# Kernel optimization log

Measured on AMD Instinct MI355X. Metric: run time of the kernel, lower is better.

The kernel has to match this reference:

```python
import jax, jax.numpy as jnp
import numpy as np

EPS = 1e-12
B, H, W, DIN = 32, 32, 32, 1024
DE = 64          # embedding_dim
K = 8192         # num_embeddings
S = 16           # code_seq_len -> 4x4 adaptive pool grid
GH = GW = 4


def setup_inputs() -> dict:
    key = jax.random.key(0)
    ks = jax.random.split(key, 8)
    return {
        "features_t0": jax.random.normal(ks[0], (B, H, W, DIN), dtype=jnp.float32),
        "features_t1": jax.random.normal(ks[1], (B, H, W, DIN), dtype=jnp.float32),
        "noise": jax.random.normal(ks[2], (B * S, DE), dtype=jnp.float32),
        "codebooks": jax.random.normal(ks[3], (K, DE), dtype=jnp.float32),
        "W_in": jax.random.normal(ks[4], (DE, DIN), dtype=jnp.float32) / np.sqrt(DIN),
        "b_in": jnp.zeros((DE,), dtype=jnp.float32),
        "W_out": jax.random.normal(ks[5], (DIN, DE), dtype=jnp.float32) / np.sqrt(DE),
        "b_out": jnp.zeros((DIN,), dtype=jnp.float32),
    }


def reference(features_t0, features_t1, noise, codebooks, W_in, b_in, W_out, b_out):
    # ---- encode: delta -> project_in -> adaptive avg pool (4x4 exact block mean) ----
    delta = features_t1 - features_t0                      # [B,H,W,DIN]
    x = jnp.einsum("bhwc,dc->bhwd", delta, W_in) + b_in    # [B,H,W,DE]
    x = x.reshape(B, GH, H // GH, GW, W // GW, DE).mean(axis=(2, 4))  # [B,4,4,DE]
    encoded = x.reshape(B, S, DE)
    flat = encoded.reshape(B * S, DE)                      # [N,DE]

    # ---- quantize (NSVQ, training mode) ----
    dist = (jnp.sum(flat**2, axis=1, keepdims=True)
            - 2.0 * flat @ codebooks.T
            + jnp.sum(codebooks**2, axis=1)[None, :])      # [N,K]
    min_idx = jnp.argmin(dist, axis=1)                     # [N]
    hard = codebooks[min_idx]                              # [N,DE]

    resid_norm = jnp.sqrt(jnp.sum((flat - hard) ** 2, axis=1, keepdims=True))
    noise_norm = jnp.sqrt(jnp.sum(noise**2, axis=1, keepdims=True))
    quantized = flat + (resid_norm / (noise_norm + EPS)) * noise  # [N,DE]

    counts = jnp.zeros((K,), dtype=jnp.float32).at[min_idx].add(1.0)
    avg_probs = counts / (B * S)
    perplexity = jnp.exp(-jnp.sum(avg_probs * jnp.log(avg_probs + EPS)))
    codebooks_used = counts.astype(jnp.int32)

    # ---- decode: [B,S,DE] -> [B,DE,4,4] -> bilinear upsample -> project_out ----
    spatial = quantized.reshape(B, GH, GW, DE).transpose(0, 3, 1, 2)  # [B,DE,4,4]
    up = jax.image.resize(spatial, (B, DE, H, W), method="bilinear")  # align_corners=False
    up = up.transpose(0, 2, 3, 1)                                     # [B,H,W,DE]
    decoded = jnp.einsum("bhwd,cd->bhwc", up, W_out) + b_out          # [B,H,W,DIN]

    indices = min_idx.reshape(B, S)
    return decoded, perplexity, codebooks_used, indices
```

## Files before the change

kernel.cpp:

```cpp
#include <hip/hip_runtime.h>
#include <math.h>

#define DIN  1024
#define DE   64
#define KK   8192
#define NN   512
#define EPSF 1e-12f

#define OUT_PERP   33554432
#define OUT_COUNTS 33554433
#define OUT_IDX    33562625

#define WS_PPOOL 0
#define WS_Y     0
#define WS_CT    1048576
#define WS_WIT   1572864
#define WS_WOT   1638400
#define WS_F     1703936
#define WS_FN    1736704
#define WS_CBN   1737216
#define WS_MIN   1745408

typedef unsigned long long ull;

__global__ __launch_bounds__(256) void k_prep(
    const float* __restrict__ t0, const float* __restrict__ t1,
    const float* __restrict__ codebooks,
    const float* __restrict__ W_in, const float* __restrict__ W_out,
    float* __restrict__ ws, float* __restrict__ counts)
{
  int t = threadIdx.x;
  int bx = blockIdx.x;
  if (bx < 1024) {
    int n = bx >> 1, h = bx & 1;
    int b = n >> 4, gi = (n >> 2) & 3, gj = n & 3;
    size_t base = (((size_t)b * 32 + gi * 8 + h * 4) * 32 + gj * 8) * DIN;
    const float4* p0 = (const float4*)(t0 + base) + t;
    const float4* p1 = (const float4*)(t1 + base) + t;
    float ax = 0.f, ay = 0.f, az = 0.f, aw = 0.f;
    #pragma unroll 2
    for (int r = 0; r < 4; ++r) {
      #pragma unroll
      for (int c = 0; c < 8; ++c) {
        size_t off = ((size_t)r * 32 + c) * (DIN / 4);
        float4 u = p1[off];
        float4 v = p0[off];
        ax += u.x - v.x; ay += u.y - v.y; az += u.z - v.z; aw += u.w - v.w;
      }
    }
    float4* pp4 = (float4*)(ws + WS_PPOOL);
    pp4[((size_t)h * NN + n) * (DIN / 4) + t] = make_float4(ax, ay, az, aw);
    return;
  }
  if (bx < 1056) {
    int bb = bx - 1024;
    int k = bb * 256 + t;
    const float* row = codebooks + (size_t)k * DE;
    float* CT = ws + WS_CT;
    float s = 0.f;
    #pragma unroll 8
    for (int d = 0; d < DE; ++d) {
      float v = row[d];
      CT[(size_t)d * KK + k] = v;
      s = fmaf(v, v, s);
    }
    (ws + WS_CBN)[k] = s;
    float* WiT = ws + WS_WIT;
    float* WoT = ws + WS_WOT;
    #pragma unroll
    for (int i = 0; i < 8; ++i) {
      int f = bb * 2048 + i * 256 + t;
      float vi = W_in[f];
      int d = f >> 10, c = f & 1023;
      WiT[c * DE + d] = vi;
      float vo = W_out[f];
      int c2 = f >> 6, d2 = f & 63;
      WoT[d2 * DIN + c2] = vo;
    }
    return;
  }
  for (int i = t; i < KK; i += 256) counts[i] = 0.f;
  ull* mb = (ull*)(ws + WS_MIN);
  for (int i = t; i < NN; i += 256) mb[i] = ~0ull;
}

__global__ __launch_bounds__(256) void k_enc(
    const float* __restrict__ ws_ro, const float* __restrict__ b_in,
    float* __restrict__ ws)
{
  __shared__ float s_pool[DIN];
  __shared__ float s_part[4][DE];
  int t = threadIdx.x;
  int n = blockIdx.x;
  const float4* pp4 = (const float4*)(ws_ro + WS_PPOOL);
  float4 a = pp4[(size_t)n * (DIN / 4) + t];
  float4 b = pp4[((size_t)NN + n) * (DIN / 4) + t];
  const float inv = 1.f / 64.f;
  ((float4*)s_pool)[t] = make_float4((a.x + b.x) * inv, (a.y + b.y) * inv,
                                     (a.z + b.z) * inv, (a.w + b.w) * inv);
  __syncthreads();
  int w = t >> 6, lane = t & 63;
  const float* WiT = ws_ro + WS_WIT;
  float acc = 0.f;
  #pragma unroll 4
  for (int i = 0; i < 256; ++i) {
    float wv = WiT[(size_t)(w * 256 + i) * DE + lane];
    acc = fmaf(wv, s_pool[w * 256 + i], acc);
  }
  s_part[w][lane] = acc;
  __syncthreads();
  if (t < DE) {
    float f = s_part[0][t] + s_part[1][t] + s_part[2][t] + s_part[3][t] + b_in[t];
    (ws + WS_F)[(size_t)n * DE + t] = f;
    float sq = f * f;
    #pragma unroll
    for (int m = 32; m > 0; m >>= 1) sq += __shfl_xor(sq, m, 64);
    if (t == 0) (ws + WS_FN)[n] = sq;
  }
}

__device__ __forceinline__ void upd_min(ull& best, float e, int k) {
  e = fmaxf(e, 0.f);
  ull p = ((ull)__float_as_uint(e) << 32) | (unsigned int)k;
  best = (p < best) ? p : best;
}

__global__ __launch_bounds__(256) void k_dist(
    const float* __restrict__ ws_ro, float* __restrict__ ws)
{
  __shared__ float4 s_f4[4][16];
  __shared__ float s_fn[4];
  __shared__ ull s_min[4];
  int t = threadIdx.x;
  int rg = blockIdx.x & 127, kc = blockIdx.x >> 7;
  int n0 = rg * 4;
  if (t < 64) {
    int r = t >> 4, g = t & 15;
    s_f4[r][g] = ((const float4*)(ws_ro + WS_F + (size_t)(n0 + r) * DE))[g];
  }
  if (t < 4) { s_fn[t] = (ws_ro + WS_FN)[n0 + t]; s_min[t] = ~0ull; }
  __syncthreads();

  int kq = (kc << 8) + t;
  int k0 = kq * 4;
  const float4* CT4 = (const float4*)(ws_ro + WS_CT);
  float4 acc0 = {0, 0, 0, 0}, acc1 = {0, 0, 0, 0}, acc2 = {0, 0, 0, 0}, acc3 = {0, 0, 0, 0};
  #pragma unroll 4
  for (int g = 0; g < 16; ++g) {
    float fa0[4], fa1[4], fa2[4], fa3[4];
    *(float4*)fa0 = s_f4[0][g];
    *(float4*)fa1 = s_f4[1][g];
    *(float4*)fa2 = s_f4[2][g];
    *(float4*)fa3 = s_f4[3][g];
    #pragma unroll
    for (int j = 0; j < 4; ++j) {
      float4 ct = CT4[(size_t)(4 * g + j) * (KK / 4) + kq];
      acc0.x = fmaf(fa0[j], ct.x, acc0.x); acc0.y = fmaf(fa0[j], ct.y, acc0.y);
      acc0.z = fmaf(fa0[j], ct.z, acc0.z); acc0.w = fmaf(fa0[j], ct.w, acc0.w);
      acc1.x = fmaf(fa1[j], ct.x, acc1.x); acc1.y = fmaf(fa1[j], ct.y, acc1.y);
      acc1.z = fmaf(fa1[j], ct.z, acc1.z); acc1.w = fmaf(fa1[j], ct.w, acc1.w);
      acc2.x = fmaf(fa2[j], ct.x, acc2.x); acc2.y = fmaf(fa2[j], ct.y, acc2.y);
      acc2.z = fmaf(fa2[j], ct.z, acc2.z); acc2.w = fmaf(fa2[j], ct.w, acc2.w);
      acc3.x = fmaf(fa3[j], ct.x, acc3.x); acc3.y = fmaf(fa3[j], ct.y, acc3.y);
      acc3.z = fmaf(fa3[j], ct.z, acc3.z); acc3.w = fmaf(fa3[j], ct.w, acc3.w);
    }
  }
  float4 cn = ((const float4*)(ws_ro + WS_CBN))[kq];
  ull b0 = ~0ull, b1 = ~0ull, b2 = ~0ull, b3 = ~0ull;
  float fn0 = s_fn[0], fn1 = s_fn[1], fn2 = s_fn[2], fn3 = s_fn[3];
  upd_min(b0, fmaf(-2.f, acc0.x, fn0 + cn.x), k0);
  upd_min(b0, fmaf(-2.f, acc0.y, fn0 + cn.y), k0 + 1);
  upd_min(b0, fmaf(-2.f, acc0.z, fn0 + cn.z), k0 + 2);
  upd_min(b0, fmaf(-2.f, acc0.w, fn0 + cn.w), k0 + 3);
  upd_min(b1, fmaf(-2.f, acc1.x, fn1 + cn.x), k0);
  upd_min(b1, fmaf(-2.f, acc1.y, fn1 + cn.y), k0 + 1);
  upd_min(b1, fmaf(-2.f, acc1.z, fn1 + cn.z), k0 + 2);
  upd_min(b1, fmaf(-2.f, acc1.w, fn1 + cn.w), k0 + 3);
  upd_min(b2, fmaf(-2.f, acc2.x, fn2 + cn.x), k0);
  upd_min(b2, fmaf(-2.f, acc2.y, fn2 + cn.y), k0 + 1);
  upd_min(b2, fmaf(-2.f, acc2.z, fn2 + cn.z), k0 + 2);
  upd_min(b2, fmaf(-2.f, acc2.w, fn2 + cn.w), k0 + 3);
  upd_min(b3, fmaf(-2.f, acc3.x, fn3 + cn.x), k0);
  upd_min(b3, fmaf(-2.f, acc3.y, fn3 + cn.y), k0 + 1);
  upd_min(b3, fmaf(-2.f, acc3.z, fn3 + cn.z), k0 + 2);
  upd_min(b3, fmaf(-2.f, acc3.w, fn3 + cn.w), k0 + 3);
  atomicMin(&s_min[0], b0);
  atomicMin(&s_min[1], b1);
  atomicMin(&s_min[2], b2);
  atomicMin(&s_min[3], b3);
  __syncthreads();
  if (t < 4) atomicMin((ull*)(ws + WS_MIN) + n0 + t, s_min[t]);
}

__global__ __launch_bounds__(256) void k_nsvq_out(
    const float* __restrict__ ws_ro, const float* __restrict__ noise,
    const float* __restrict__ codebooks, const float* __restrict__ b_out,
    float* __restrict__ ws, float* __restrict__ counts,
    float* __restrict__ idx_out)
{
  __shared__ float s_q[DE];
  int t = threadIdx.x;
  int n = blockIdx.x;
  if (t < DE) {
    ull m = ((const ull*)(ws_ro + WS_MIN))[n];
    unsigned idx = (unsigned)(m & 0xffffffffu);
    float f = (ws_ro + WS_F)[(size_t)n * DE + t];
    float hv = codebooks[(size_t)idx * DE + t];
    float nz = noise[(size_t)n * DE + t];
    float df = f - hv;
    float sd = df * df, sn = nz * nz;
    #pragma unroll
    for (int m2 = 32; m2 > 0; m2 >>= 1) {
      sd += __shfl_xor(sd, m2, 64);
      sn += __shfl_xor(sn, m2, 64);
    }
    float scale = sqrtf(sd) / (sqrtf(sn) + EPSF);
    s_q[t] = fmaf(scale, nz, f);
    if (t == 0) {
      idx_out[n] = (float)idx;
      atomicAdd(&counts[idx], 1.0f);
    }
  }
  __syncthreads();
  const float4* WoT4 = (const float4*)(ws_ro + WS_WOT);
  float4 acc = {0, 0, 0, 0};
  #pragma unroll 4
  for (int i = 0; i < DE; ++i) {
    float q = s_q[i];
    float4 w = WoT4[(size_t)i * (DIN / 4) + t];
    acc.x = fmaf(q, w.x, acc.x); acc.y = fmaf(q, w.y, acc.y);
    acc.z = fmaf(q, w.z, acc.z); acc.w = fmaf(q, w.w, acc.w);
  }
  float4 bo = ((const float4*)b_out)[t];
  acc.x += bo.x; acc.y += bo.y; acc.z += bo.z; acc.w += bo.w;
  ((float4*)(ws + WS_Y))[(size_t)n * (DIN / 4) + t] = acc;
}

__global__ __launch_bounds__(256) void k_decode(
    const float* __restrict__ ws_ro, const float* __restrict__ counts,
    float* __restrict__ decoded, float* __restrict__ perp)
{
  int t = threadIdx.x;
  if (blockIdx.x == 1024) {
    __shared__ float red[256];
    float s = 0.f;
    for (int k = t; k < KK; k += 256) {
      float p = counts[k] * (1.0f / 512.0f);
      s += p * logf(p + EPSF);
    }
    red[t] = s;
    __syncthreads();
    for (int o = 128; o > 0; o >>= 1) {
      if (t < o) red[t] += red[t + o];
      __syncthreads();
    }
    if (t == 0) perp[0] = expf(-red[0]);
    return;
  }
  __shared__ float s_y[8][DIN];
  const float* Y = ws_ro + WS_Y;
  int bh = blockIdx.x;
  int b = bh >> 5, h = bh & 31;
  float sy = (h + 0.5f) * 0.125f - 0.5f;
  int y0 = (int)floorf(sy);
  float fy = sy - (float)y0;
  int y1 = min(y0 + 1, 3);
  y0 = max(y0, 0);
  #pragma unroll
  for (int gx = 0; gx < 4; ++gx) {
    ((float4*)s_y[gx])[t]     = ((const float4*)(Y + (size_t)(b * 16 + y0 * 4 + gx) * DIN))[t];
    ((float4*)s_y[4 + gx])[t] = ((const float4*)(Y + (size_t)(b * 16 + y1 * 4 + gx) * DIN))[t];
  }
  __syncthreads();
  float4* ob = (float4*)(decoded + (size_t)bh * (32 * DIN));
  for (int w = 0; w < 32; ++w) {
    float sx = (w + 0.5f) * 0.125f - 0.5f;
    int x0 = (int)floorf(sx);
    float fx = sx - (float)x0;
    int x1 = min(x0 + 1, 3);
    x0 = max(x0, 0);
    float w00 = (1.f - fy) * (1.f - fx), w01 = (1.f - fy) * fx;
    float w10 = fy * (1.f - fx), w11 = fy * fx;
    float4 v00 = ((const float4*)s_y[x0])[t];
    float4 v01 = ((const float4*)s_y[x1])[t];
    float4 v10 = ((const float4*)s_y[4 + x0])[t];
    float4 v11 = ((const float4*)s_y[4 + x1])[t];
    float4 o;
    o.x = w00 * v00.x + w01 * v01.x + w10 * v10.x + w11 * v11.x;
    o.y = w00 * v00.y + w01 * v01.y + w10 * v10.y + w11 * v11.y;
    o.z = w00 * v00.z + w01 * v01.z + w10 * v10.z + w11 * v11.z;
    o.w = w00 * v00.w + w01 * v01.w + w10 * v10.w + w11 * v11.w;
    ob[(size_t)w * (DIN / 4) + t] = o;
  }
}

extern "C" void kernel_launch(void* const* d_in, const int* in_sizes, int n_in,
                              void* d_out, int out_size, void* d_ws, size_t ws_size,
                              hipStream_t stream) {
  const float* t0        = (const float*)d_in[0];
  const float* t1        = (const float*)d_in[1];
  const float* noise     = (const float*)d_in[2];
  const float* codebooks = (const float*)d_in[3];
  const float* W_in      = (const float*)d_in[4];
  const float* b_in      = (const float*)d_in[5];
  const float* W_out     = (const float*)d_in[6];
  const float* b_out     = (const float*)d_in[7];
  float* out = (float*)d_out;
  float* ws  = (float*)d_ws;

  float* decoded = out;
  float* perp    = out + OUT_PERP;
  float* counts  = out + OUT_COUNTS;
  float* idx_out = out + OUT_IDX;

  hipLaunchKernelGGL(k_prep, dim3(1057), dim3(256), 0, stream,
                     t0, t1, codebooks, W_in, W_out, ws, counts);
  hipLaunchKernelGGL(k_enc, dim3(512), dim3(256), 0, stream,
                     ws, b_in, ws);
  hipLaunchKernelGGL(k_dist, dim3(1024), dim3(256), 0, stream,
                     ws, ws);
  hipLaunchKernelGGL(k_nsvq_out, dim3(512), dim3(256), 0, stream,
                     ws, noise, codebooks, b_out, ws, counts, idx_out);
  hipLaunchKernelGGL(k_decode, dim3(1025), dim3(256), 0, stream,
                     ws, counts, decoded, perp);
}
```

Before: 419.3 us.

## Split pooling reduction across channel quarters with batched loads and in-block combine

The pooling stage now launches four blocks per pooled cell, each covering a quarter of the channels. Its four wavefronts each take two rows of pixels, and the partial sums are combined in shared memory. Loads are batched eight at a time to raise memory-level parallelism, and the encoder reads a single pooled vector instead of two halves. The goal is more concurrent blocks and more outstanding loads on the bandwidth-bound read of both feature tensors, at the cost of a block sync and a shared-memory reduction.

```diff
diff --git a/kernel.cpp b/kernel.cpp
--- a/kernel.cpp
+++ b/kernel.cpp
@@ -31,29 +31,44 @@
 {
   int t = threadIdx.x;
   int bx = blockIdx.x;
-  if (bx < 1024) {
-    int n = bx >> 1, h = bx & 1;
+  if (bx < 2048) {
+    __shared__ float4 s_p[4][64];
+    int n = bx >> 2, q = bx & 3;
     int b = n >> 4, gi = (n >> 2) & 3, gj = n & 3;
-    size_t base = (((size_t)b * 32 + gi * 8 + h * 4) * 32 + gj * 8) * DIN;
-    const float4* p0 = (const float4*)(t0 + base) + t;
-    const float4* p1 = (const float4*)(t1 + base) + t;
+    int pg = t >> 6, ch = t & 63;
+    size_t pix0 = (((size_t)b * 32 + gi * 8 + pg * 2) * 32) + gj * 8;
+    const float4* p0 = (const float4*)t0 + pix0 * (DIN / 4) + q * 64 + ch;
+    const float4* p1 = (const float4*)t1 + pix0 * (DIN / 4) + q * 64 + ch;
     float ax = 0.f, ay = 0.f, az = 0.f, aw = 0.f;
-    #pragma unroll 2
-    for (int r = 0; r < 4; ++r) {
+    #pragma unroll
+    for (int half = 0; half < 2; ++half) {
+      float4 u[8], v[8];
       #pragma unroll
-      for (int c = 0; c < 8; ++c) {
-        size_t off = ((size_t)r * 32 + c) * (DIN / 4);
-        float4 u = p1[off];
-        float4 v = p0[off];
-        ax += u.x - v.x; ay += u.y - v.y; az += u.z - v.z; aw += u.w - v.w;
+      for (int i = 0; i < 8; ++i) {
+        size_t off = ((size_t)half * 32 + i) * (DIN / 4);
+        u[i] = p1[off];
+        v[i] = p0[off];
       }
-    }
-    float4* pp4 = (float4*)(ws + WS_PPOOL);
-    pp4[((size_t)h * NN + n) * (DIN / 4) + t] = make_float4(ax, ay, az, aw);
+      #pragma unroll
+      for (int i = 0; i < 8; ++i) {
+        ax += u[i].x - v[i].x; ay += u[i].y - v[i].y;
+        az += u[i].z - v[i].z; aw += u[i].w - v[i].w;
+      }
+    }
+    s_p[pg][ch] = make_float4(ax, ay, az, aw);
+    __syncthreads();
+    if (t < 64) {
+      float4 a0 = s_p[0][t], a1 = s_p[1][t], a2 = s_p[2][t], a3 = s_p[3][t];
+      ((float4*)(ws + WS_PPOOL))[(size_t)n * (DIN / 4) + q * 64 + t] =
+          make_float4(a0.x + a1.x + a2.x + a3.x,
+                      a0.y + a1.y + a2.y + a3.y,
+                      a0.z + a1.z + a2.z + a3.z,
+                      a0.w + a1.w + a2.w + a3.w);
+    }
     return;
   }
-  if (bx < 1056) {
-    int bb = bx - 1024;
+  if (bx < 2080) {
+    int bb = bx - 2048;
     int k = bb * 256 + t;
     const float* row = codebooks + (size_t)k * DE;
     float* CT = ws + WS_CT;
@@ -92,12 +107,10 @@
   __shared__ float s_part[4][DE];
   int t = threadIdx.x;
   int n = blockIdx.x;
-  const float4* pp4 = (const float4*)(ws_ro + WS_PPOOL);
-  float4 a = pp4[(size_t)n * (DIN / 4) + t];
-  float4 b = pp4[((size_t)NN + n) * (DIN / 4) + t];
+  const float4* pool4 = (const float4*)(ws_ro + WS_PPOOL);
+  float4 a = pool4[(size_t)n * (DIN / 4) + t];
   const float inv = 1.f / 64.f;
-  ((float4*)s_pool)[t] = make_float4((a.x + b.x) * inv, (a.y + b.y) * inv,
-                                     (a.z + b.z) * inv, (a.w + b.w) * inv);
+  ((float4*)s_pool)[t] = make_float4(a.x * inv, a.y * inv, a.z * inv, a.w * inv);
   __syncthreads();
   int w = t >> 6, lane = t & 63;
   const float* WiT = ws_ro + WS_WIT;
@@ -313,7 +326,7 @@
   float* counts  = out + OUT_COUNTS;
   float* idx_out = out + OUT_IDX;
 
-  hipLaunchKernelGGL(k_prep, dim3(1057), dim3(256), 0, stream,
+  hipLaunchKernelGGL(k_prep, dim3(2081), dim3(256), 0, stream,
                      t0, t1, codebooks, W_in, W_out, ws, counts);
   hipLaunchKernelGGL(k_enc, dim3(512), dim3(256), 0, stream,
                      ws, b_in, ws);
```

Result: no change. 413.3 us (-1.4%).
